# Kernel tuning notes

Measured on AMD Instinct MI355X. Metric: run time of the kernel, lower is better.

## Reference

```python
import jax, jax.numpy as jnp
import numpy as np

B, T, DIM = 2, 2048, 1024
HID = 4096
H, KVH, HD = 16, 4, 64
WIN = 512
NORM_EPS = 1e-5
QK_EPS = 1e-6
LS_INIT = 0.01


def setup_inputs() -> dict:
    key = jax.random.key(0)
    ks = jax.random.split(key, 12)
    s = lambda fan_in: 1.0 / np.sqrt(fan_in)
    return {
        "x": jax.random.normal(ks[0], (B, T, DIM), jnp.float32),
        # torch Linear weights are (out, in); y = x @ W.T
        "wq": jax.random.normal(ks[1], (H * HD, DIM), jnp.float32) * s(DIM),
        "wk": jax.random.normal(ks[2], (KVH * HD, DIM), jnp.float32) * s(DIM),
        "wv": jax.random.normal(ks[3], (KVH * HD, DIM), jnp.float32) * s(DIM),
        "wo": jax.random.normal(ks[4], (DIM, H * HD), jnp.float32) * s(H * HD),
        "w1": jax.random.normal(ks[5], (HID, DIM), jnp.float32) * s(DIM),
        "w2": jax.random.normal(ks[6], (DIM, HID), jnp.float32) * s(HID),
        "w3": jax.random.normal(ks[7], (HID, DIM), jnp.float32) * s(DIM),
        "q_norm_w": jnp.ones((HD,), jnp.float32),
        "k_norm_w": jnp.ones((HD,), jnp.float32),
        "attn_norm_w": jnp.ones((DIM,), jnp.float32),
        "ffn_norm_w": jnp.ones((DIM,), jnp.float32),
        "attn_scale": jnp.full((DIM,), LS_INIT, jnp.float32),
        "ffn_scale": jnp.full((DIM,), LS_INIT, jnp.float32),
    }


def _rmsnorm(x, w, eps):
    return x * jax.lax.rsqrt(jnp.mean(x * x, axis=-1, keepdims=True) + eps) * w


def _attention(x, wq, wk, wv, wo, q_norm_w, k_norm_w):
    b, t, _ = x.shape
    q = (x @ wq.T).reshape(b, t, H, HD)
    k = (x @ wk.T).reshape(b, t, KVH, HD)
    v = (x @ wv.T).reshape(b, t, KVH, HD)
    q = _rmsnorm(q, q_norm_w, QK_EPS)
    k = _rmsnorm(k, k_norm_w, QK_EPS)
    # GQA: repeat kv heads to H heads
    rep = H // KVH
    k = jnp.repeat(k, rep, axis=2)  # (b,t,H,HD)
    v = jnp.repeat(v, rep, axis=2)
    scale = 1.0 / np.sqrt(HD)
    scores = jnp.einsum("bqhd,bkhd->bhqk", q, k) * scale  # (b,H,t,t)
    row = jnp.arange(t)[:, None]
    col = jnp.arange(t)[None, :]
    mask = (row >= col) & (row - col < WIN)  # (t,t) bool
    scores = jnp.where(mask[None, None], scores, -jnp.inf)
    probs = jax.nn.softmax(scores, axis=-1)
    y = jnp.einsum("bhqk,bkhd->bqhd", probs, v).reshape(b, t, H * HD)
    return y @ wo.T


def reference(x, wq, wk, wv, wo, w1, w2, w3, q_norm_w, k_norm_w,
              attn_norm_w, ffn_norm_w, attn_scale, ffn_scale):
    r = _attention(_rmsnorm(x, attn_norm_w, NORM_EPS), wq, wk, wv, wo,
                   q_norm_w, k_norm_w)
    h = x + r * attn_scale
    hn = _rmsnorm(h, ffn_norm_w, NORM_EPS)
    ffn = (jax.nn.silu(hn @ w1.T) * (hn @ w3.T)) @ w2.T
    return h + ffn * ffn_scale
```

## Files before the change

kernel.cpp:

```cpp
#include <hip/hip_runtime.h>

typedef unsigned short u16;
typedef unsigned int u32;
typedef unsigned char u8;
typedef short bf16x8 __attribute__((ext_vector_type(8)));
typedef float f32x4 __attribute__((ext_vector_type(4)));
typedef float f32x16 __attribute__((ext_vector_type(16)));
typedef int i32x4 __attribute__((ext_vector_type(4)));
typedef int i32x8 __attribute__((ext_vector_type(8)));

#define AS1 __attribute__((address_space(1)))
#define AS3 __attribute__((address_space(3)))

#define B_ 2
#define T_ 2048
#define DIM_ 1024
#define HID_ 4096
#define H_ 16
#define KVH_ 4
#define HD_ 64
#define WIN_ 512

#define SCALE_A 0x7C7C7C7C
#define SCALE_B 0x79797979

__device__ __forceinline__ u16 f2bf(float f) {
    union { float f; u32 u; } v; v.f = f;
    u32 r = v.u + 0x7FFFu + ((v.u >> 16) & 1u);
    return (u16)(r >> 16);
}
__device__ __forceinline__ float bf2f(u32 u) {
    union { u32 u; float f; } v; v.u = u << 16;
    return v.f;
}
__device__ __forceinline__ float4 ld4bf(const u16* p) {
    uint2 u = *(const uint2*)p;
    float4 r;
    r.x = bf2f(u.x & 0xFFFFu); r.y = bf2f(u.x >> 16);
    r.z = bf2f(u.y & 0xFFFFu); r.w = bf2f(u.y >> 16);
    return r;
}
__device__ __forceinline__ void load_lds16(const void* g, void* l) {
    __builtin_amdgcn_global_load_lds((AS1 void*)(g), (AS3 void*)(l), 16, 0, 0);
}
#define WAITBAR(N) asm volatile("s_waitcnt vmcnt(" #N ")\n\ts_barrier" ::: "memory")

__global__ __launch_bounds__(256) void mega_cvt(const float* __restrict__ wq,
                                                const float* __restrict__ wk,
                                                const float* __restrict__ wv,
                                                const float* __restrict__ wo,
                                                const float* __restrict__ w1,
                                                const float* __restrict__ w3,
                                                const float* __restrict__ w2,
                                                u16* __restrict__ wqkv,
                                                u16* __restrict__ wo_b,
                                                u8* __restrict__ w13_8,
                                                u8* __restrict__ w2_8) {
    int i = blockIdx.x * 256 + threadIdx.x;
    if (i < 655360) {
        const float* s; uint2* dbase; size_t didx;
        if (i < 262144)      { s = wq + (size_t)i * 4; dbase = (uint2*)wqkv; didx = i; }
        else if (i < 327680) { int f = i - 262144; s = wk + (size_t)f * 4; dbase = (uint2*)wqkv; didx = 262144 + f; }
        else if (i < 393216) { int f = i - 327680; s = wv + (size_t)f * 4; dbase = (uint2*)wqkv; didx = 327680 + f; }
        else                 { int f = i - 393216; s = wo + (size_t)f * 4; dbase = (uint2*)wo_b; didx = f; }
        float4 v = *(const float4*)s;
        u32 lo = (u32)f2bf(v.x) | ((u32)f2bf(v.y) << 16);
        u32 hi = (u32)f2bf(v.z) | ((u32)f2bf(v.w) << 16);
        dbase[didx] = make_uint2(lo, hi);
    } else {
        const float* s; u32* dbase; size_t didx;
        if (i < 1703936)      { int f = i - 655360;  int c = f >> 8; int n = (c >> 5) * 64 + (c & 31);
                                s = w1 + (size_t)f * 4; dbase = (u32*)w13_8; didx = (size_t)n * 256 + (f & 255); }
        else if (i < 2752512) { int f = i - 1703936; int c = f >> 8; int n = (c >> 5) * 64 + 32 + (c & 31);
                                s = w3 + (size_t)f * 4; dbase = (u32*)w13_8; didx = (size_t)n * 256 + (f & 255); }
        else                  { int f = i - 2752512; s = w2 + (size_t)f * 4; dbase = (u32*)w2_8; didx = f; }
        float4 v = *(const float4*)s;
        int p = __builtin_amdgcn_cvt_pk_fp8_f32(v.x * 64.f, v.y * 64.f, 0, false);
        p = __builtin_amdgcn_cvt_pk_fp8_f32(v.z * 64.f, v.w * 64.f, p, true);
        dbase[didx] = (u32)p;
    }
}

__global__ __launch_bounds__(256) void rmsnorm_kernel(const float* __restrict__ x,
                                                      const float* __restrict__ w,
                                                      u16* __restrict__ out, float eps) {
    int row = blockIdx.x, tid = threadIdx.x;
    const float4 v = ((const float4*)(x + (size_t)row * DIM_))[tid];
    float ss = v.x * v.x + v.y * v.y + v.z * v.z + v.w * v.w;
#pragma unroll
    for (int m = 1; m < 64; m <<= 1) ss += __shfl_xor(ss, m);
    __shared__ float part[4];
    if ((tid & 63) == 0) part[tid >> 6] = ss;
    __syncthreads();
    float tot = part[0] + part[1] + part[2] + part[3];
    float r = rsqrtf(tot * (1.0f / DIM_) + eps);
    const float4 wv = ((const float4*)w)[tid];
    u32 lo = (u32)f2bf(v.x * r * wv.x) | ((u32)f2bf(v.y * r * wv.y) << 16);
    u32 hi = (u32)f2bf(v.z * r * wv.z) | ((u32)f2bf(v.w * r * wv.w) << 16);
    ((uint2*)(out + (size_t)row * DIM_))[tid] = make_uint2(lo, hi);
}

__global__ __launch_bounds__(256) void fuse_attn_kernel(const float* __restrict__ x,
                                                        const u16* __restrict__ p,
                                                        const float* __restrict__ ascale,
                                                        const float* __restrict__ fnw,
                                                        float* __restrict__ h,
                                                        u8* __restrict__ xn8) {
    int row = blockIdx.x, tid = threadIdx.x;
    const float4 xv = ((const float4*)(x + (size_t)row * DIM_))[tid];
    float4 a0 = ld4bf(p + (size_t)row * DIM_ + tid * 4);
    float4 a1 = ld4bf(p + 4194304 + (size_t)row * DIM_ + tid * 4);
    const float4 sc = ((const float4*)ascale)[tid];
    float4 hv;
    hv.x = xv.x + (a0.x + a1.x) * sc.x;
    hv.y = xv.y + (a0.y + a1.y) * sc.y;
    hv.z = xv.z + (a0.z + a1.z) * sc.z;
    hv.w = xv.w + (a0.w + a1.w) * sc.w;
    ((float4*)(h + (size_t)row * DIM_))[tid] = hv;
    float ss = hv.x * hv.x + hv.y * hv.y + hv.z * hv.z + hv.w * hv.w;
#pragma unroll
    for (int m = 1; m < 64; m <<= 1) ss += __shfl_xor(ss, m);
    __shared__ float part[4];
    if ((tid & 63) == 0) part[tid >> 6] = ss;
    __syncthreads();
    float tot = part[0] + part[1] + part[2] + part[3];
    float r = rsqrtf(tot * (1.0f / DIM_) + 1e-5f) * 8.0f;
    const float4 wv = ((const float4*)fnw)[tid];
    int pk = __builtin_amdgcn_cvt_pk_fp8_f32(hv.x * r * wv.x, hv.y * r * wv.y, 0, false);
    pk = __builtin_amdgcn_cvt_pk_fp8_f32(hv.z * r * wv.z, hv.w * r * wv.w, pk, true);
    ((u32*)xn8)[(size_t)row * 256 + tid] = (u32)pk;
}

__global__ __launch_bounds__(256) void fuse_ffn_kernel(const float* __restrict__ h,
                                                       const u16* __restrict__ p,
                                                       const float* __restrict__ fscale,
                                                       float* __restrict__ out) {
    int row = blockIdx.x, tid = threadIdx.x;
    const float4 hv = ((const float4*)(h + (size_t)row * DIM_))[tid];
    size_t off = (size_t)row * DIM_ + tid * 4;
    float4 a0 = ld4bf(p + off);
    float4 a1 = ld4bf(p + 4194304 + off);
    float4 a2 = ld4bf(p + 8388608 + off);
    float4 a3 = ld4bf(p + 12582912 + off);
    const float4 sc = ((const float4*)fscale)[tid];
    float4 o;
    o.x = hv.x + (a0.x + a1.x + a2.x + a3.x) * sc.x;
    o.y = hv.y + (a0.y + a1.y + a2.y + a3.y) * sc.y;
    o.z = hv.z + (a0.z + a1.z + a2.z + a3.z) * sc.z;
    o.w = hv.w + (a0.w + a1.w + a2.w + a3.w) * sc.w;
    ((float4*)(out + (size_t)row * DIM_))[tid] = o;
}

__global__ __launch_bounds__(256) void qkv_post_kernel(const u16* __restrict__ qkv,
                                                       const float* __restrict__ qw,
                                                       const float* __restrict__ kw,
                                                       u16* __restrict__ Qb,
                                                       u16* __restrict__ Kb,
                                                       u16* __restrict__ Vb) {
    int bt = blockIdx.x;
    int b = bt >> 11, t = bt & (T_ - 1);
    int wave = threadIdx.x >> 6, lane = threadIdx.x & 63;
    const u16* row0 = qkv + (size_t)bt * 1536;
    const u16* row1 = row0 + 6291456;
    float qwl = qw[lane], kwl = kw[lane];
#pragma unroll
    for (int i = 0; i < 4; i++) {
        int h = wave * 4 + i;
        float v = bf2f(row0[h * 64 + lane]) + bf2f(row1[h * 64 + lane]);
        float ss = v * v;
#pragma unroll
        for (int m = 1; m < 64; m <<= 1) ss += __shfl_xor(ss, m);
        float r = rsqrtf(ss * (1.0f / 64.0f) + 1e-6f);
        Qb[(((size_t)(b * H_ + h)) * T_ + t) * HD_ + lane] = f2bf(v * r * qwl);
    }
    {
        float v = bf2f(row0[1024 + wave * 64 + lane]) + bf2f(row1[1024 + wave * 64 + lane]);
        float ss = v * v;
#pragma unroll
        for (int m = 1; m < 64; m <<= 1) ss += __shfl_xor(ss, m);
        float r = rsqrtf(ss * (1.0f / 64.0f) + 1e-6f);
        Kb[(((size_t)(b * KVH_ + wave)) * T_ + t) * HD_ + lane] = f2bf(v * r * kwl);
        float vv = bf2f(row0[1280 + wave * 64 + lane]) + bf2f(row1[1280 + wave * 64 + lane]);
        Vb[(((size_t)(b * KVH_ + wave)) * T_ + t) * HD_ + lane] = f2bf(vv);
    }
}

__global__ __launch_bounds__(256) void vtrans_kernel(const u16* __restrict__ Vb,
                                                     u16* __restrict__ Vt) {
    const int bk = blockIdx.x >> 5;
    const int t0 = (blockIdx.x & 31) * 64;
    const int tid = threadIdx.x;
    __shared__ __align__(16) u16 tile[64][64];
    const u16* src = Vb + ((size_t)bk * T_ + t0) * HD_;
#pragma unroll
    for (int i = 0; i < 2; i++) {
        int g = tid + i * 256;
        int r = g >> 3, c8 = g & 7;
        *(bf16x8*)&tile[r][c8 * 8] = *(const bf16x8*)(src + (size_t)r * HD_ + c8 * 8);
    }
    __syncthreads();
    const int d = tid >> 2, ts = (tid & 3) * 16;
    u16 buf[16];
#pragma unroll
    for (int j = 0; j < 16; j++) buf[j] = tile[ts + j][d];
    u16* dst = Vt + (size_t)bk * HD_ * T_ + (size_t)d * T_ + t0 + ts;
    *(bf16x8*)(dst) = *(const bf16x8*)&buf[0];
    *(bf16x8*)(dst + 8) = *(const bf16x8*)&buf[8];
}

__global__ __launch_bounds__(512, 2) void flash_kernel(const u16* __restrict__ Qb,
                                                       const u16* __restrict__ Kb,
                                                       const u16* __restrict__ Vt,
                                                       u16* __restrict__ Ob) {
    const int b = blockIdx.z, kvh = blockIdx.y, qt = blockIdx.x;
    const int q0 = qt * 64;
    const int tid = threadIdx.x, wave = tid >> 6, lane = tid & 63;
    const int head = wave & 3, qhalf = wave >> 2;
    const int h = kvh * 4 + head;
    const int m = lane & 15, quad = lane >> 4;

    __shared__ __align__(16) u16 Ks[2][4096];
    __shared__ __align__(16) u16 Vs[2][4096];
    __shared__ __align__(16) u16 Ps[8][16 * 72];

    const u16* Qp = Qb + ((size_t)(b * H_ + h) * T_) * HD_;
    const u16* Kp = Kb + ((size_t)(b * KVH_ + kvh) * T_) * HD_;
    const u16* Vp = Vt + ((size_t)(b * KVH_ + kvh) * HD_) * T_;

    const int qbase = q0 + qhalf * 32;
    bf16x8 qa[2][2];
#pragma unroll
    for (int qs = 0; qs < 2; qs++) {
        const u16* qp = Qp + (size_t)(qbase + qs * 16 + m) * 64 + quad * 8;
        qa[qs][0] = *(const bf16x8*)(qp);
        qa[qs][1] = *(const bf16x8*)(qp + 32);
    }

    f32x4 o[2][4] = {};
    float mrun[2] = {-1e30f, -1e30f}, lrun[2] = {0.f, 0.f};

    const int kt0 = (q0 >= WIN_) ? ((q0 - (WIN_ - 1)) >> 6) : 0;
    const int kt1 = qt;

    const int srow = tid >> 3;
    const int schunk = (tid & 7) ^ (srow & 7);
    const u16* Ksrc = Kp + (size_t)srow * 64 + schunk * 8;
    const u16* Vsrc = Vp + (size_t)srow * T_ + schunk * 8;
    const int ldsOff = wave * 512;

    load_lds16(Ksrc + (size_t)kt0 * 4096, &Ks[0][ldsOff]);
    load_lds16(Vsrc + kt0 * 64, &Vs[0][ldsOff]);

    for (int kt = kt0; kt <= kt1; ++kt) {
        const int kbase = kt << 6;
        const int cur = (kt - kt0) & 1;
        if (kt < kt1) {
            load_lds16(Ksrc + (size_t)(kt + 1) * 4096, &Ks[cur ^ 1][ldsOff]);
            load_lds16(Vsrc + (kt + 1) * 64, &Vs[cur ^ 1][ldsOff]);
            WAITBAR(2);
        } else {
            WAITBAR(0);
        }
        bf16x8 kf[4][2], vb[4][2];
#pragma unroll
        for (int st = 0; st < 4; st++) {
            const int r64 = (st * 16 + m) * 64;
#pragma unroll
            for (int hf = 0; hf < 2; hf++) {
                const int c = (((hf << 2) + quad) ^ (m & 7)) * 8;
                kf[st][hf] = *(const bf16x8*)&Ks[cur][r64 + c];
                vb[st][hf] = *(const bf16x8*)&Vs[cur][r64 + c];
            }
        }
#pragma unroll
        for (int qs = 0; qs < 2; qs++) {
            const int qlo_s = qbase + qs * 16;
            if (kbase <= qlo_s + 15 && kbase >= qlo_s - 574) {
                f32x4 s4[4];
#pragma unroll
                for (int st = 0; st < 4; st++) {
                    f32x4 z = {0.f, 0.f, 0.f, 0.f};
                    z = __builtin_amdgcn_mfma_f32_16x16x32_bf16(kf[st][0], qa[qs][0], z, 0, 0, 0);
                    z = __builtin_amdgcn_mfma_f32_16x16x32_bf16(kf[st][1], qa[qs][1], z, 0, 0, 0);
                    s4[st] = z;
                }
                float v[16];
                const bool full = (kbase + 63 <= qlo_s) && (kbase >= qlo_s - 496);
                if (full) {
#pragma unroll
                    for (int i = 0; i < 16; i++) v[i] = s4[i >> 2][i & 3] * 0.125f;
                } else {
                    const int D = qlo_s + m - kbase - quad * 4;
#pragma unroll
                    for (int st = 0; st < 4; st++)
#pragma unroll
                        for (int r = 0; r < 4; r++) {
                            int diff = D - st * 16 - r;
                            v[st * 4 + r] = ((u32)diff < (u32)WIN_) ? s4[st][r] * 0.125f : -INFINITY;
                        }
                }
                float t0 = fmaxf(fmaxf(fmaxf(v[0], v[1]), fmaxf(v[2], v[3])),
                                 fmaxf(fmaxf(v[4], v[5]), fmaxf(v[6], v[7])));
                float t1 = fmaxf(fmaxf(fmaxf(v[8], v[9]), fmaxf(v[10], v[11])),
                                 fmaxf(fmaxf(v[12], v[13]), fmaxf(v[14], v[15])));
                float rmax = fmaxf(t0, t1);
                rmax = fmaxf(rmax, __shfl_xor(rmax, 16));
                rmax = fmaxf(rmax, __shfl_xor(rmax, 32));
                float mnew = fmaxf(mrun[qs], rmax);
                float alpha = __expf(mrun[qs] - mnew);
                float p[16];
#pragma unroll
                for (int i = 0; i < 16; i++) p[i] = __expf(v[i] - mnew);
                float u0 = ((p[0] + p[1]) + (p[2] + p[3])) + ((p[4] + p[5]) + (p[6] + p[7]));
                float u1 = ((p[8] + p[9]) + (p[10] + p[11])) + ((p[12] + p[13]) + (p[14] + p[15]));
                float psum = u0 + u1;
                psum += __shfl_xor(psum, 16);
                psum += __shfl_xor(psum, 32);
                lrun[qs] = lrun[qs] * alpha + psum;
                mrun[qs] = mnew;
#pragma unroll
                for (int d = 0; d < 4; d++) {
                    o[qs][d][0] *= alpha; o[qs][d][1] *= alpha;
                    o[qs][d][2] *= alpha; o[qs][d][3] *= alpha;
                }
#pragma unroll
                for (int st = 0; st < 4; st++) {
                    u32 lo = (u32)f2bf(p[st * 4 + 0]) | ((u32)f2bf(p[st * 4 + 1]) << 16);
                    u32 hi = (u32)f2bf(p[st * 4 + 2]) | ((u32)f2bf(p[st * 4 + 3]) << 16);
                    *(uint2*)&Ps[wave][m * 72 + st * 16 + quad * 4] = make_uint2(lo, hi);
                }
                bf16x8 pa0 = *(const bf16x8*)&Ps[wave][m * 72 + quad * 8];
                bf16x8 pa1 = *(const bf16x8*)&Ps[wave][m * 72 + 32 + quad * 8];
#pragma unroll
                for (int d = 0; d < 4; d++) {
                    o[qs][d] = __builtin_amdgcn_mfma_f32_16x16x32_bf16(vb[d][0], pa0, o[qs][d], 0, 0, 0);
                    o[qs][d] = __builtin_amdgcn_mfma_f32_16x16x32_bf16(vb[d][1], pa1, o[qs][d], 0, 0, 0);
                }
            }
        }
        asm volatile("s_barrier" ::: "memory");
    }
#pragma unroll
    for (int qs = 0; qs < 2; qs++) {
        float inv = 1.0f / lrun[qs];
        u16* ob = Ob + ((size_t)(b * T_ + qbase + qs * 16 + m)) * (H_ * HD_) + h * HD_;
#pragma unroll
        for (int d = 0; d < 4; d++) {
            u32 lo = (u32)f2bf(o[qs][d][0] * inv) | ((u32)f2bf(o[qs][d][1] * inv) << 16);
            u32 hi = (u32)f2bf(o[qs][d][2] * inv) | ((u32)f2bf(o[qs][d][3] * inv) << 16);
            *(uint2*)(ob + d * 16 + quad * 4) = make_uint2(lo, hi);
        }
    }
}

__global__ __launch_bounds__(256) void gemm_bt(const u16* __restrict__ A,
                                               const u16* __restrict__ Bt,
                                               u16* __restrict__ Cb,
                                               int M, int N, int K, int KS) {
    __shared__ __align__(16) u16 As[2][4096];
    __shared__ __align__(16) u16 Bs[2][4096];
    const int tid = threadIdx.x, wave = tid >> 6, lane = tid & 63;
    const int m = lane & 15, quad = lane >> 4;
    const int m0 = blockIdx.y * 128, n0 = blockIdx.x * 128;
    const int wm = (wave >> 1) * 64, wn = (wave & 1) * 64;
    const int kb = blockIdx.z * KS;
    const int nIter = KS >> 5;
    const int slot = wave * 2;
    const int flat0 = slot * 512 + lane * 8;
    const int row0_ = flat0 >> 5, col0 = flat0 & 31;
    const int flat1 = (slot + 1) * 512 + lane * 8;
    const int row1_ = flat1 >> 5, col1 = flat1 & 31;

    f32x4 acc[4][4] = {};

    load_lds16(A + (size_t)(m0 + row0_) * K + kb + col0, &As[0][slot * 512]);
    load_lds16(Bt + (size_t)(n0 + row0_) * K + kb + col0, &Bs[0][slot * 512]);
    load_lds16(A + (size_t)(m0 + row1_) * K + kb + col1, &As[0][(slot + 1) * 512]);
    load_lds16(Bt + (size_t)(n0 + row1_) * K + kb + col1, &Bs[0][(slot + 1) * 512]);

    for (int it = 0; it < nIter; ++it) {
        __syncthreads();
        const int cur = it & 1;
        if (it + 1 < nIter) {
            const int nb = 1 - cur;
            const int k0 = kb + (it + 1) * 32;
            load_lds16(A + (size_t)(m0 + row0_) * K + k0 + col0, &As[nb][slot * 512]);
            load_lds16(Bt + (size_t)(n0 + row0_) * K + k0 + col0, &Bs[nb][slot * 512]);
            load_lds16(A + (size_t)(m0 + row1_) * K + k0 + col1, &As[nb][(slot + 1) * 512]);
            load_lds16(Bt + (size_t)(n0 + row1_) * K + k0 + col1, &Bs[nb][(slot + 1) * 512]);
        }
        bf16x8 af[4], bfr[4];
#pragma unroll
        for (int i = 0; i < 4; i++) af[i] = *(const bf16x8*)&As[cur][(wm + i * 16 + m) * 32 + quad * 8];
#pragma unroll
        for (int j = 0; j < 4; j++) bfr[j] = *(const bf16x8*)&Bs[cur][(wn + j * 16 + m) * 32 + quad * 8];
#pragma unroll
        for (int i = 0; i < 4; i++)
#pragma unroll
            for (int j = 0; j < 4; j++)
                acc[i][j] = __builtin_amdgcn_mfma_f32_16x16x32_bf16(af[i], bfr[j], acc[i][j], 0, 0, 0);
    }

    u16* Cz = Cb + (size_t)blockIdx.z * M * N;
#pragma unroll
    for (int i = 0; i < 4; i++) {
        int rowb = m0 + wm + i * 16 + quad * 4;
#pragma unroll
        for (int j = 0; j < 4; j++) {
            int col = n0 + wn + j * 16 + m;
#pragma unroll
            for (int r = 0; r < 4; r++)
                Cz[(size_t)(rowb + r) * N + col] = f2bf(acc[i][j][r]);
        }
    }
}

#define MFMA8(a, b, c) __builtin_amdgcn_mfma_scale_f32_32x32x64_f8f6f4(a, b, c, 0, 0, 0, SCALE_A, 0, SCALE_B)
#define PHASE_MFMA(I0, I1)                           \
    __builtin_amdgcn_s_setprio(1);                   \
    acc[I0][0] = MFMA8(a0, bf0, acc[I0][0]);         \
    acc[I0][1] = MFMA8(a0, bf1, acc[I0][1]);         \
    acc[I1][0] = MFMA8(a1, bf0, acc[I1][0]);         \
    acc[I1][1] = MFMA8(a1, bf1, acc[I1][1]);         \
    __builtin_amdgcn_s_setprio(0);

template <int MODE>
__global__ __launch_bounds__(512) void gemm_fp8(const u8* __restrict__ A,
                                                const u8* __restrict__ Bt,
                                                u16* __restrict__ Cb,
                                                u8* __restrict__ C8,
                                                int M, int N, int K, int KS) {
    __shared__ __align__(16) u8 As[2][32768];
    __shared__ __align__(16) u8 Bs[2][32768];
    const int tid = threadIdx.x, wave = tid >> 6, lane = tid & 63;
    const int l31 = lane & 31, lh = lane >> 5;
    const int m0 = blockIdx.y * 256, n0 = blockIdx.x * 256;
    const int wm = (wave >> 2) * 128, wn = (wave & 3) * 64;
    const int kb = blockIdx.z * KS;
    const int KT = KS >> 7;

    const u8* Ab = A + (size_t)m0 * K;
    const u8* Bb = Bt + (size_t)n0 * K;

    auto STAGE = [&](const u8* src, int kk, int h, u8* lds) {
#pragma unroll
        for (int p = 0; p < 2; p++) {
            const int s = p * 512 + tid;
            const int r = (h << 7) + (s >> 3);
            const int c = (s & 7) ^ (r & 7);
            load_lds16(src + (size_t)r * K + kk + c * 16,
                       lds + (h << 14) + (p << 13) + (wave << 10));
        }
    };
    auto FRAG = [&](const u8* t, int ks, int row) -> i32x8 {
        const int c0 = ks * 4 + (lh << 1);
        const u8* rp = t + row * 128;
        union { i32x4 h[2]; i32x8 v; } u;
        u.h[0] = *(const i32x4*)(rp + ((c0 ^ (row & 7)) << 4));
        u.h[1] = *(const i32x4*)(rp + (((c0 + 1) ^ (row & 7)) << 4));
        return u.v;
    };

    f32x16 acc[4][2] = {};

    STAGE(Ab, kb, 0, As[0]);
    STAGE(Ab, kb, 1, As[0]);
    STAGE(Bb, kb, 0, Bs[0]);
    STAGE(Bb, kb, 1, Bs[0]);

    for (int kt = 0; kt < KT; ++kt) {
        const int cur = kt & 1;
        if (kt + 1 < KT) {
            asm volatile("s_barrier" ::: "memory");
            const int kn = kb + (kt + 1) * 128;
            STAGE(Ab, kn, 0, As[1 - cur]);
            STAGE(Ab, kn, 1, As[1 - cur]);
            STAGE(Bb, kn, 0, Bs[1 - cur]);
            STAGE(Bb, kn, 1, Bs[1 - cur]);
            WAITBAR(8);
        } else {
            WAITBAR(0);
        }
        const u8* Ac = As[cur];
        const u8* Bc = Bs[cur];
        i32x8 bf0, bf1, a0, a1;
#pragma unroll
        for (int ks = 0; ks < 2; ks++) {
            bf0 = FRAG(Bc, ks, wn + l31);
            bf1 = FRAG(Bc, ks, wn + 32 + l31);
            a0 = FRAG(Ac, ks, wm + l31);
            a1 = FRAG(Ac, ks, wm + 32 + l31);
            PHASE_MFMA(0, 1)
            a0 = FRAG(Ac, ks, wm + 64 + l31);
            a1 = FRAG(Ac, ks, wm + 96 + l31);
            PHASE_MFMA(2, 3)
        }
    }

    if (MODE == 0) {
        u16* Cz = Cb + (size_t)blockIdx.z * M * N;
#pragma unroll
        for (int i = 0; i < 4; i++)
#pragma unroll
            for (int j = 0; j < 2; j++) {
                int col = n0 + wn + j * 32 + l31;
#pragma unroll
                for (int reg = 0; reg < 16; reg++) {
                    int row = m0 + wm + i * 32 + (reg & 3) + 8 * (reg >> 2) + 4 * lh;
                    Cz[(size_t)row * N + col] = f2bf(acc[i][j][reg]);
                }
            }
    } else {
        int c = (n0 >> 1) + (wn >> 1) + l31;
#pragma unroll
        for (int i = 0; i < 4; i++)
#pragma unroll
            for (int reg = 0; reg < 16; reg++) {
                int row = m0 + wm + i * 32 + (reg & 3) + 8 * (reg >> 2) + 4 * lh;
                float g1 = acc[i][0][reg], g3 = acc[i][1][reg];
                float res = (g1 / (1.f + __expf(-g1))) * g3 * 8.0f;
                int p = __builtin_amdgcn_cvt_pk_fp8_f32(res, res, 0, false);
                C8[(size_t)row * (N >> 1) + c] = (u8)(p & 0xFF);
            }
    }
}

extern "C" void kernel_launch(void* const* d_in, const int* in_sizes, int n_in,
                              void* d_out, int out_size, void* d_ws, size_t ws_size,
                              hipStream_t stream) {
    const float* x = (const float*)d_in[0];
    const float* wq = (const float*)d_in[1];
    const float* wk = (const float*)d_in[2];
    const float* wv = (const float*)d_in[3];
    const float* wo = (const float*)d_in[4];
    const float* w1 = (const float*)d_in[5];
    const float* w2 = (const float*)d_in[6];
    const float* w3 = (const float*)d_in[7];
    const float* qnw = (const float*)d_in[8];
    const float* knw = (const float*)d_in[9];
    const float* anw = (const float*)d_in[10];
    const float* fnw = (const float*)d_in[11];
    const float* ascale = (const float*)d_in[12];
    const float* fscale = (const float*)d_in[13];
    float* out = (float*)d_out;

    char* ws = (char*)d_ws;
    u16* wqkv_bf = (u16*)(ws + 0);
    u16* wo_bf = (u16*)(ws + 3145728);
    u8* w13_8 = (u8*)(ws + 5242880);
    u8* w2_8 = (u8*)(ws + 13631488);
    u16* xn_bf = (u16*)(ws + 17825792);
    u8* xn8 = (u8*)(ws + 26214400);
    float* h_f = (float*)(ws + 30408704);
    char* P = ws + 47185920;
    u16* qkv_part = (u16*)(P + 0);
    u16* Qb = (u16*)(P + 25165824);
    u16* Kb = (u16*)(P + 33554432);
    u16* Vb = (u16*)(P + 35651584);
    u16* att_bf = (u16*)(P + 37748736);
    u16* Vt = (u16*)(P + 46137344);
    u16* wo_part = (u16*)(P + 0);
    u8* gsw8 = (u8*)(P + 16777216);
    u16* w2_part = (u16*)(P + 33554432);

    mega_cvt<<<14848, 256, 0, stream>>>(wq, wk, wv, wo, w1, w3, w2,
                                        wqkv_bf, wo_bf, w13_8, w2_8);
    rmsnorm_kernel<<<4096, 256, 0, stream>>>(x, anw, xn_bf, 1e-5f);
    gemm_bt<<<dim3(12, 32, 2), 256, 0, stream>>>(xn_bf, wqkv_bf, qkv_part,
                                                 4096, 1536, 1024, 512);
    qkv_post_kernel<<<4096, 256, 0, stream>>>(qkv_part, qnw, knw, Qb, Kb, Vb);
    vtrans_kernel<<<256, 256, 0, stream>>>(Vb, Vt);
    flash_kernel<<<dim3(32, KVH_, B_), 512, 0, stream>>>(Qb, Kb, Vt, att_bf);
    gemm_bt<<<dim3(8, 32, 2), 256, 0, stream>>>(att_bf, wo_bf, wo_part,
                                                4096, 1024, 1024, 512);
    fuse_attn_kernel<<<4096, 256, 0, stream>>>(x, wo_part, ascale, fnw, h_f, xn8);
    gemm_fp8<1><<<dim3(32, 16, 1), 512, 0, stream>>>(xn8, w13_8, nullptr, gsw8,
                                                     4096, 8192, 1024, 1024);
    gemm_fp8<0><<<dim3(4, 16, 4), 512, 0, stream>>>(gsw8, w2_8, w2_part, nullptr,
                                                    4096, 1024, 4096, 1024);
    fuse_ffn_kernel<<<4096, 256, 0, stream>>>(h_f, w2_part, fscale, out);
}
```

Measured before the change: 306.2 us.

## Move QKV and output projections from bf16 to scaled fp8 MFMA GEMMs

Converts wq/wk/wv/wo weights to fp8 instead of bf16, makes the attention rmsnorm and flash output emit fp8 (with a power-of-two prescale), and runs the QKV and output projections through the existing gemm_fp8 kernel instead of the bf16 gemm_bt. The output projection now uses a 4-way K split, so fuse_attn sums four partials. This aims to halve operand bytes and use the higher-throughput fp8 MFMA path, at the cost of reduced precision in the attention projections and extra partial-sum traffic.

```diff
diff --git a/kernel.cpp b/kernel.cpp
--- a/kernel.cpp
+++ b/kernel.cpp
@@ -52,38 +52,33 @@
                                                 const float* __restrict__ w1,
                                                 const float* __restrict__ w3,
                                                 const float* __restrict__ w2,
-                                                u16* __restrict__ wqkv,
-                                                u16* __restrict__ wo_b,
+                                                u8* __restrict__ wqkv8,
+                                                u8* __restrict__ wo8,
                                                 u8* __restrict__ w13_8,
                                                 u8* __restrict__ w2_8) {
     int i = blockIdx.x * 256 + threadIdx.x;
+    const float* s; u32* dbase; size_t didx;
     if (i < 655360) {
-        const float* s; uint2* dbase; size_t didx;
-        if (i < 262144)      { s = wq + (size_t)i * 4; dbase = (uint2*)wqkv; didx = i; }
-        else if (i < 327680) { int f = i - 262144; s = wk + (size_t)f * 4; dbase = (uint2*)wqkv; didx = 262144 + f; }
-        else if (i < 393216) { int f = i - 327680; s = wv + (size_t)f * 4; dbase = (uint2*)wqkv; didx = 327680 + f; }
-        else                 { int f = i - 393216; s = wo + (size_t)f * 4; dbase = (uint2*)wo_b; didx = f; }
-        float4 v = *(const float4*)s;
-        u32 lo = (u32)f2bf(v.x) | ((u32)f2bf(v.y) << 16);
-        u32 hi = (u32)f2bf(v.z) | ((u32)f2bf(v.w) << 16);
-        dbase[didx] = make_uint2(lo, hi);
+        if (i < 262144)      { s = wq + (size_t)i * 4; dbase = (u32*)wqkv8; didx = i; }
+        else if (i < 327680) { int f = i - 262144; s = wk + (size_t)f * 4; dbase = (u32*)wqkv8; didx = 262144 + f; }
+        else if (i < 393216) { int f = i - 327680; s = wv + (size_t)f * 4; dbase = (u32*)wqkv8; didx = 327680 + f; }
+        else                 { int f = i - 393216; s = wo + (size_t)f * 4; dbase = (u32*)wo8; didx = f; }
     } else {
-        const float* s; u32* dbase; size_t didx;
         if (i < 1703936)      { int f = i - 655360;  int c = f >> 8; int n = (c >> 5) * 64 + (c & 31);
                                 s = w1 + (size_t)f * 4; dbase = (u32*)w13_8; didx = (size_t)n * 256 + (f & 255); }
         else if (i < 2752512) { int f = i - 1703936; int c = f >> 8; int n = (c >> 5) * 64 + 32 + (c & 31);
                                 s = w3 + (size_t)f * 4; dbase = (u32*)w13_8; didx = (size_t)n * 256 + (f & 255); }
         else                  { int f = i - 2752512; s = w2 + (size_t)f * 4; dbase = (u32*)w2_8; didx = f; }
-        float4 v = *(const float4*)s;
-        int p = __builtin_amdgcn_cvt_pk_fp8_f32(v.x * 64.f, v.y * 64.f, 0, false);
-        p = __builtin_amdgcn_cvt_pk_fp8_f32(v.z * 64.f, v.w * 64.f, p, true);
-        dbase[didx] = (u32)p;
-    }
+    }
+    float4 v = *(const float4*)s;
+    int p = __builtin_amdgcn_cvt_pk_fp8_f32(v.x * 64.f, v.y * 64.f, 0, false);
+    p = __builtin_amdgcn_cvt_pk_fp8_f32(v.z * 64.f, v.w * 64.f, p, true);
+    dbase[didx] = (u32)p;
 }
 
 __global__ __launch_bounds__(256) void rmsnorm_kernel(const float* __restrict__ x,
                                                       const float* __restrict__ w,
-                                                      u16* __restrict__ out, float eps) {
+                                                      u8* __restrict__ out, float eps) {
     int row = blockIdx.x, tid = threadIdx.x;
     const float4 v = ((const float4*)(x + (size_t)row * DIM_))[tid];
     float ss = v.x * v.x + v.y * v.y + v.z * v.z + v.w * v.w;
@@ -93,11 +88,11 @@
     if ((tid & 63) == 0) part[tid >> 6] = ss;
     __syncthreads();
     float tot = part[0] + part[1] + part[2] + part[3];
-    float r = rsqrtf(tot * (1.0f / DIM_) + eps);
+    float r = rsqrtf(tot * (1.0f / DIM_) + eps) * 8.0f;
     const float4 wv = ((const float4*)w)[tid];
-    u32 lo = (u32)f2bf(v.x * r * wv.x) | ((u32)f2bf(v.y * r * wv.y) << 16);
-    u32 hi = (u32)f2bf(v.z * r * wv.z) | ((u32)f2bf(v.w * r * wv.w) << 16);
-    ((uint2*)(out + (size_t)row * DIM_))[tid] = make_uint2(lo, hi);
+    int pk = __builtin_amdgcn_cvt_pk_fp8_f32(v.x * r * wv.x, v.y * r * wv.y, 0, false);
+    pk = __builtin_amdgcn_cvt_pk_fp8_f32(v.z * r * wv.z, v.w * r * wv.w, pk, true);
+    ((u32*)out)[(size_t)row * 256 + tid] = (u32)pk;
 }
 
 __global__ __launch_bounds__(256) void fuse_attn_kernel(const float* __restrict__ x,
@@ -108,14 +103,17 @@
                                                         u8* __restrict__ xn8) {
     int row = blockIdx.x, tid = threadIdx.x;
     const float4 xv = ((const float4*)(x + (size_t)row * DIM_))[tid];
-    float4 a0 = ld4bf(p + (size_t)row * DIM_ + tid * 4);
-    float4 a1 = ld4bf(p + 4194304 + (size_t)row * DIM_ + tid * 4);
+    size_t off = (size_t)row * DIM_ + tid * 4;
+    float4 a0 = ld4bf(p + off);
+    float4 a1 = ld4bf(p + 4194304 + off);
+    float4 a2 = ld4bf(p + 8388608 + off);
+    float4 a3 = ld4bf(p + 12582912 + off);
     const float4 sc = ((const float4*)ascale)[tid];
     float4 hv;
-    hv.x = xv.x + (a0.x + a1.x) * sc.x;
-    hv.y = xv.y + (a0.y + a1.y) * sc.y;
-    hv.z = xv.z + (a0.z + a1.z) * sc.z;
-    hv.w = xv.w + (a0.w + a1.w) * sc.w;
+    hv.x = xv.x + (a0.x + a1.x + a2.x + a3.x) * sc.x;
+    hv.y = xv.y + (a0.y + a1.y + a2.y + a3.y) * sc.y;
+    hv.z = xv.z + (a0.z + a1.z + a2.z + a3.z) * sc.z;
+    hv.w = xv.w + (a0.w + a1.w + a2.w + a3.w) * sc.w;
     ((float4*)(h + (size_t)row * DIM_))[tid] = hv;
     float ss = hv.x * hv.x + hv.y * hv.y + hv.z * hv.z + hv.w * hv.w;
 #pragma unroll
@@ -211,7 +209,7 @@
 __global__ __launch_bounds__(512, 2) void flash_kernel(const u16* __restrict__ Qb,
                                                        const u16* __restrict__ Kb,
                                                        const u16* __restrict__ Vt,
-                                                       u16* __restrict__ Ob) {
+                                                       u8* __restrict__ Ob8) {
     const int b = blockIdx.z, kvh = blockIdx.y, qt = blockIdx.x;
     const int q0 = qt * 64;
     const int tid = threadIdx.x, wave = tid >> 6, lane = tid & 63;
@@ -342,75 +340,13 @@
     }
 #pragma unroll
     for (int qs = 0; qs < 2; qs++) {
-        float inv = 1.0f / lrun[qs];
-        u16* ob = Ob + ((size_t)(b * T_ + qbase + qs * 16 + m)) * (H_ * HD_) + h * HD_;
+        float inv = 8.0f / lrun[qs];
+        u8* ob = Ob8 + ((size_t)(b * T_ + qbase + qs * 16 + m)) * (H_ * HD_) + h * HD_;
 #pragma unroll
         for (int d = 0; d < 4; d++) {
-            u32 lo = (u32)f2bf(o[qs][d][0] * inv) | ((u32)f2bf(o[qs][d][1] * inv) << 16);
-            u32 hi = (u32)f2bf(o[qs][d][2] * inv) | ((u32)f2bf(o[qs][d][3] * inv) << 16);
-            *(uint2*)(ob + d * 16 + quad * 4) = make_uint2(lo, hi);
-        }
-    }
-}
-
-__global__ __launch_bounds__(256) void gemm_bt(const u16* __restrict__ A,
-                                               const u16* __restrict__ Bt,
-                                               u16* __restrict__ Cb,
-                                               int M, int N, int K, int KS) {
-    __shared__ __align__(16) u16 As[2][4096];
-    __shared__ __align__(16) u16 Bs[2][4096];
-    const int tid = threadIdx.x, wave = tid >> 6, lane = tid & 63;
-    const int m = lane & 15, quad = lane >> 4;
-    const int m0 = blockIdx.y * 128, n0 = blockIdx.x * 128;
-    const int wm = (wave >> 1) * 64, wn = (wave & 1) * 64;
-    const int kb = blockIdx.z * KS;
-    const int nIter = KS >> 5;
-    const int slot = wave * 2;
-    const int flat0 = slot * 512 + lane * 8;
-    const int row0_ = flat0 >> 5, col0 = flat0 & 31;
-    const int flat1 = (slot + 1) * 512 + lane * 8;
-    const int row1_ = flat1 >> 5, col1 = flat1 & 31;
-
-    f32x4 acc[4][4] = {};
-
-    load_lds16(A + (size_t)(m0 + row0_) * K + kb + col0, &As[0][slot * 512]);
-    load_lds16(Bt + (size_t)(n0 + row0_) * K + kb + col0, &Bs[0][slot * 512]);
-    load_lds16(A + (size_t)(m0 + row1_) * K + kb + col1, &As[0][(slot + 1) * 512]);
-    load_lds16(Bt + (size_t)(n0 + row1_) * K + kb + col1, &Bs[0][(slot + 1) * 512]);
-
-    for (int it = 0; it < nIter; ++it) {
-        __syncthreads();
-        const int cur = it & 1;
-        if (it + 1 < nIter) {
-            const int nb = 1 - cur;
-            const int k0 = kb + (it + 1) * 32;
-            load_lds16(A + (size_t)(m0 + row0_) * K + k0 + col0, &As[nb][slot * 512]);
-            load_lds16(Bt + (size_t)(n0 + row0_) * K + k0 + col0, &Bs[nb][slot * 512]);
-            load_lds16(A + (size_t)(m0 + row1_) * K + k0 + col1, &As[nb][(slot + 1) * 512]);
-            load_lds16(Bt + (size_t)(n0 + row1_) * K + k0 + col1, &Bs[nb][(slot + 1) * 512]);
-        }
-        bf16x8 af[4], bfr[4];
-#pragma unroll
-        for (int i = 0; i < 4; i++) af[i] = *(const bf16x8*)&As[cur][(wm + i * 16 + m) * 32 + quad * 8];
-#pragma unroll
-        for (int j = 0; j < 4; j++) bfr[j] = *(const bf16x8*)&Bs[cur][(wn + j * 16 + m) * 32 + quad * 8];
-#pragma unroll
-        for (int i = 0; i < 4; i++)
-#pragma unroll
-            for (int j = 0; j < 4; j++)
-                acc[i][j] = __builtin_amdgcn_mfma_f32_16x16x32_bf16(af[i], bfr[j], acc[i][j], 0, 0, 0);
-    }
-
-    u16* Cz = Cb + (size_t)blockIdx.z * M * N;
-#pragma unroll
-    for (int i = 0; i < 4; i++) {
-        int rowb = m0 + wm + i * 16 + quad * 4;
-#pragma unroll
-        for (int j = 0; j < 4; j++) {
-            int col = n0 + wn + j * 16 + m;
-#pragma unroll
-            for (int r = 0; r < 4; r++)
-                Cz[(size_t)(rowb + r) * N + col] = f2bf(acc[i][j][r]);
+            int pk = __builtin_amdgcn_cvt_pk_fp8_f32(o[qs][d][0] * inv, o[qs][d][1] * inv, 0, false);
+            pk = __builtin_amdgcn_cvt_pk_fp8_f32(o[qs][d][2] * inv, o[qs][d][3] * inv, pk, true);
+            *(u32*)(ob + d * 16 + quad * 4) = (u32)pk;
         }
     }
 }
@@ -545,11 +481,11 @@
     float* out = (float*)d_out;
 
     char* ws = (char*)d_ws;
-    u16* wqkv_bf = (u16*)(ws + 0);
-    u16* wo_bf = (u16*)(ws + 3145728);
+    u8* wqkv8 = (u8*)(ws + 0);
+    u8* wo8 = (u8*)(ws + 1572864);
     u8* w13_8 = (u8*)(ws + 5242880);
     u8* w2_8 = (u8*)(ws + 13631488);
-    u16* xn_bf = (u16*)(ws + 17825792);
+    u8* xq8 = (u8*)(ws + 17825792);
     u8* xn8 = (u8*)(ws + 26214400);
     float* h_f = (float*)(ws + 30408704);
     char* P = ws + 47185920;
@@ -557,22 +493,22 @@
     u16* Qb = (u16*)(P + 25165824);
     u16* Kb = (u16*)(P + 33554432);
     u16* Vb = (u16*)(P + 35651584);
-    u16* att_bf = (u16*)(P + 37748736);
+    u8* att8 = (u8*)(P + 37748736);
     u16* Vt = (u16*)(P + 46137344);
     u16* wo_part = (u16*)(P + 0);
     u8* gsw8 = (u8*)(P + 16777216);
     u16* w2_part = (u16*)(P + 33554432);
 
     mega_cvt<<<14848, 256, 0, stream>>>(wq, wk, wv, wo, w1, w3, w2,
-                                        wqkv_bf, wo_bf, w13_8, w2_8);
-    rmsnorm_kernel<<<4096, 256, 0, stream>>>(x, anw, xn_bf, 1e-5f);
-    gemm_bt<<<dim3(12, 32, 2), 256, 0, stream>>>(xn_bf, wqkv_bf, qkv_part,
-                                                 4096, 1536, 1024, 512);
+                                        wqkv8, wo8, w13_8, w2_8);
+    rmsnorm_kernel<<<4096, 256, 0, stream>>>(x, anw, xq8, 1e-5f);
+    gemm_fp8<0><<<dim3(6, 16, 2), 512, 0, stream>>>(xq8, wqkv8, qkv_part, nullptr,
+                                                    4096, 1536, 1024, 512);
     qkv_post_kernel<<<4096, 256, 0, stream>>>(qkv_part, qnw, knw, Qb, Kb, Vb);
     vtrans_kernel<<<256, 256, 0, stream>>>(Vb, Vt);
-    flash_kernel<<<dim3(32, KVH_, B_), 512, 0, stream>>>(Qb, Kb, Vt, att_bf);
-    gemm_bt<<<dim3(8, 32, 2), 256, 0, stream>>>(att_bf, wo_bf, wo_part,
-                                                4096, 1024, 1024, 512);
+    flash_kernel<<<dim3(32, KVH_, B_), 512, 0, stream>>>(Qb, Kb, Vt, att8);
+    gemm_fp8<0><<<dim3(4, 16, 4), 512, 0, stream>>>(att8, wo8, wo_part, nullptr,
+                                                    4096, 1024, 1024, 256);
     fuse_attn_kernel<<<4096, 256, 0, stream>>>(x, wo_part, ascale, fnw, h_f, xn8);
     gemm_fp8<1><<<dim3(32, 16, 1), 512, 0, stream>>>(xn8, w13_8, nullptr, gsw8,
                                                      4096, 8192, 1024, 1024);
```

New measurement: 290.9 us. -5.0%, faster.
